# Kernel tuning notes

Hardware: AMD Instinct MI355X
Metric: run time of the kernel (lower is better)

The kernel has to match this reference:

```python
import jax, jax.numpy as jnp
import numpy as np
from jax import lax

_F1 = np.array([1., 3., 3., 1.], dtype=np.float32)
_F1 = _F1 / _F1.sum()
F2D = jnp.asarray(np.outer(_F1, _F1))  # [4,4] normalized FIR filter
LRELU_GAIN = float(np.sqrt(2.0))


def _upfirdn2d_up(x, up, pad0, pad1, gain):
    # zero-insertion upsample + pad + FIR filter (VALID depthwise conv)
    B, C, H, W = x.shape
    if up > 1:
        x = jnp.zeros((B, C, H, up, W, up), x.dtype).at[:, :, :, 0, :, 0].set(x)
        x = x.reshape(B, C, H * up, W * up)
    x = jnp.pad(x, ((0, 0), (0, 0), (pad0, pad1), (pad0, pad1)))
    k = jnp.broadcast_to((F2D * gain).astype(x.dtype), (C, 1, 4, 4))
    return lax.conv_general_dilated(x, k, (1, 1), 'VALID', feature_group_count=C)


def _affine(w, aw, ab):
    # FullyConnectedLayer: weight_gain = 1/sqrt(in_features), bias_init handled in setup
    return w @ aw.T * (1.0 / np.sqrt(aw.shape[1])) + ab


def _mod_conv(x, weight, styles, up):
    # fused modulated conv2d with demodulation, batch-as-groups trick
    B = x.shape[0]
    O, I, kh, kw = weight.shape
    w = weight[None] * styles[:, None, :, None, None]          # [B,O,I,kh,kw]
    d = lax.rsqrt(jnp.sum(jnp.square(w), axis=(2, 3, 4)) + 1e-8)  # [B,O]
    w = w * d[:, :, None, None, None]
    if up == 2:
        # conv2d_resample: FIR upsample (gain=up^2), then true conv (flipped weight)
        # padding=1, fw=4, up=2 -> px0 = 1 + (4+2-1)//2 = 3, px1 = 1 + (4-2)//2 = 2
        x = _upfirdn2d_up(x, 2, 3, 2, 4.0)
        w = w[:, :, :, ::-1, ::-1]
        pad = 'VALID'
    else:
        pad = ((kh // 2, kh // 2), (kw // 2, kw // 2))
    xr = x.reshape(1, B * I, x.shape[2], x.shape[3])
    wr = w.reshape(B * O, I, kh, kw)
    y = lax.conv_general_dilated(xr, wr, (1, 1), pad, feature_group_count=B)
    return y.reshape(B, O, y.shape[2], y.shape[3])


def _lrelu_bias(x, b, clamp=256.0):
    # bias_act: lrelu(x+b) * sqrt(2), clamp
    x = x + b[None, :, None, None]
    x = jnp.where(x >= 0, x, 0.2 * x) * LRELU_GAIN
    return jnp.clip(x, -clamp, clamp)


def setup_inputs() -> dict:
    key = jax.random.key(0)
    ks = jax.random.split(key, 12)
    B, Cin, Cout, Wd, R, IC = 8, 512, 512, 512, 64, 3
    r = R // 2
    return dict(
        x=jax.random.normal(ks[0], (B, Cin, r, r), jnp.float32),
        img=jax.random.normal(ks[1], (B, IC, r, r), jnp.float32),
        ws=jax.random.normal(ks[2], (B, 3, Wd), jnp.float32),
        a0_w=jax.random.normal(ks[3], (Cin, Wd), jnp.float32),
        a0_b=jnp.ones((Cin,), jnp.float32),
        w0=jax.random.normal(ks[4], (Cout, Cin, 3, 3), jnp.float32),
        b0=jnp.zeros((Cout,), jnp.float32),
        ns0=jnp.asarray(0.1, jnp.float32),
        nc0=jax.random.normal(ks[5], (R, R), jnp.float32),
        a1_w=jax.random.normal(ks[6], (Cout, Wd), jnp.float32),
        a1_b=jnp.ones((Cout,), jnp.float32),
        w1=jax.random.normal(ks[7], (Cout, Cout, 3, 3), jnp.float32),
        b1=jnp.zeros((Cout,), jnp.float32),
        ns1=jnp.asarray(0.1, jnp.float32),
        nc1=jax.random.normal(ks[8], (R, R), jnp.float32),
        at_w=jax.random.normal(ks[9], (Cout, Wd), jnp.float32),
        at_b=jnp.ones((Cout,), jnp.float32),
        wt=jax.random.normal(ks[10], (IC, Cout), jnp.float32),
        bt=jnp.zeros((IC,), jnp.float32),
    )


def reference(x, img, ws, a0_w, a0_b, w0, b0, ns0, nc0,
              a1_w, a1_b, w1, b1, ns1, nc1, at_w, at_b, wt, bt):
    # conv0: modulated conv, up=2, const noise, lrelu bias-act with clamp
    s0 = _affine(ws[:, 0], a0_w, a0_b)
    h = _mod_conv(x, w0, s0, up=2)
    h = h + nc0[None, None] * ns0
    h = _lrelu_bias(h, b0)
    # conv1: modulated conv, up=1
    s1 = _affine(ws[:, 1], a1_w, a1_b)
    h = _mod_conv(h, w1, s1, up=1)
    h = h + nc1[None, None] * ns1
    h = _lrelu_bias(h, b1)
    # skip architecture: upsample img (upsample2d: px0=2, px1=1, gain=4)
    img_up = _upfirdn2d_up(img, 2, 2, 1, 4.0)
    # torgb: 1x1 modulated conv, no demodulation, styles scaled by weight_gain
    st = _affine(ws[:, 2], at_w, at_b) * (1.0 / np.sqrt(wt.shape[1]))
    y = jnp.einsum('bihw,bi,oi->bohw', h, st, wt)
    y = jnp.clip(y + bt[None, :, None, None], -256.0, 256.0)
    return h, img_up + y
```

## Files before the change

### kernel.cpp

```cpp
#include <hip/hip_runtime.h>
#include <stdint.h>

typedef unsigned short u16;
typedef unsigned int   u32;

#define DEVINL __device__ __forceinline__

typedef __bf16 bf16x8 __attribute__((ext_vector_type(8)));
typedef float  f32x4  __attribute__((ext_vector_type(4)));
typedef unsigned short u16x8 __attribute__((ext_vector_type(8)));

#define RSQRT512 0.044194173824159216f
#define LRELU_G  1.4142135623730951f

DEVINL u16 f2bf(float f) {
  union { float f; u32 u; } v; v.f = f;
  u32 r = v.u + 0x7fffu + ((v.u >> 16) & 1u);
  return (u16)(r >> 16);
}
DEVINL float bf2f(u16 b) {
  union { u32 u; float f; } v; v.u = ((u32)b) << 16;
  return v.f;
}

#define AS1 __attribute__((address_space(1)))
#define AS3 __attribute__((address_space(3)))
DEVINL void gload16(const void* g, void* l) {
  __builtin_amdgcn_global_load_lds((AS1 const u32*)(uintptr_t)g,
                                   (AS3 u32*)(u32)(uintptr_t)l, 16, 0, 0);
}

__global__ __launch_bounds__(256)
void style_kernel(const float* __restrict__ wsin,
                  const float* __restrict__ a0w, const float* __restrict__ a0b,
                  const float* __restrict__ a1w, const float* __restrict__ a1b,
                  const float* __restrict__ atw, const float* __restrict__ atb,
                  float* __restrict__ s_all)
{
  int wid = threadIdx.x >> 6, lane = threadIdx.x & 63;
  int idx = blockIdx.x * 4 + wid;
  int j = idx >> 12;
  int b = (idx >> 9) & 7;
  int o = idx & 511;
  const float* A  = (j == 0) ? a0w : ((j == 1) ? a1w : atw);
  const float* Ab = (j == 0) ? a0b : ((j == 1) ? a1b : atb);
  const float* wv = wsin + (b * 3 + j) * 512;
  float p = 0.f;
  #pragma unroll
  for (int m = 0; m < 512; m += 64) p += wv[m + lane] * A[(size_t)o * 512 + m + lane];
  #pragma unroll
  for (int s = 32; s; s >>= 1) p += __shfl_xor(p, s, 64);
  if (lane == 0) {
    float v = p * RSQRT512 + Ab[o];
    if (j == 2) v *= RSQRT512;
    s_all[idx] = v;
  }
}

__global__ __launch_bounds__(256)
void demod_kernel(const float* __restrict__ w, const float* __restrict__ s_j,
                  float* __restrict__ dOut)
{
  int o = blockIdx.x;
  int t = threadIdx.x;
  __shared__ float red2[4][8];
  float part[8];
  #pragma unroll
  for (int b = 0; b < 8; ++b) part[b] = 0.f;
  #pragma unroll
  for (int hh = 0; hh < 2; ++hh) {
    int i = t + hh * 256;
    const float* wp = w + ((size_t)o * 512 + i) * 9;
    float ws = 0.f;
    #pragma unroll
    for (int k = 0; k < 9; ++k) ws += wp[k] * wp[k];
    #pragma unroll
    for (int b = 0; b < 8; ++b) {
      float sv = s_j[b * 512 + i];
      part[b] += sv * sv * ws;
    }
  }
  #pragma unroll
  for (int b = 0; b < 8; ++b)
    #pragma unroll
    for (int s = 32; s; s >>= 1) part[b] += __shfl_xor(part[b], s, 64);
  int wid = t >> 6, lane = t & 63;
  if (lane == 0) {
    #pragma unroll
    for (int b = 0; b < 8; ++b) red2[wid][b] = part[b];
  }
  __syncthreads();
  if (t < 8) {
    float d = red2[0][t] + red2[1][t] + red2[2][t] + red2[3][t];
    dOut[t * 512 + o] = 1.0f / sqrtf(d + 1e-8f);
  }
}

template <int FLIP>
__global__ __launch_bounds__(256)
void wpack_kernel(const float* __restrict__ w, const float* __restrict__ s_j,
                  const float* __restrict__ dIn, u16* __restrict__ wg)
{
  int b = blockIdx.x >> 6;
  int kq = blockIdx.x & 63;
  float sv[8];
  #pragma unroll
  for (int e = 0; e < 8; ++e) sv[e] = s_j[b * 512 + kq * 8 + e];
  int t = threadIdx.x;
  #pragma unroll 1
  for (int rep = 0; rep < 2; ++rep) {
    int o = rep * 256 + t;
    float d = dIn[b * 512 + o];
    const float* wp = w + ((size_t)o * 512 + kq * 8) * 9;
    float wv[72];
    #pragma unroll
    for (int j = 0; j < 72; ++j) wv[j] = wp[j];
    #pragma unroll
    for (int tapOut = 0; tapOut < 9; ++tapOut) {
      int ksrc = FLIP ? (8 - tapOut) : tapOut;
      u16x8 g;
      #pragma unroll
      for (int e = 0; e < 8; ++e) g[e] = f2bf(wv[e * 9 + ksrc] * sv[e] * d);
      *(u16x8*)&wg[((((size_t)(b * 9 + tapOut)) * 64 + kq) * 512 + o) * 8] = g;
    }
  }
}

__global__ __launch_bounds__(256)
void upblur_kernel(const float* __restrict__ x, u16* __restrict__ xb)
{
  int b = blockIdx.x >> 6, c8 = blockIdx.x & 63;
  __shared__ float slab[8192];
  int t = threadIdx.x;
  const float* sp = x + (((size_t)(b * 512 + c8 * 8)) << 10);
  #pragma unroll
  for (int i = 0; i < 32; ++i) slab[t + i * 256] = sp[t + i * 256];
  __syncthreads();
  u16* ob = xb + ((size_t)(b * 64 + c8)) * 34848;
  #pragma unroll 1
  for (int idx = t; idx < 4356; idx += 256) {
    int p = idx / 66;
    int q = idx - p * 66;
    int m0, m1; float wy0, wy1;
    if ((p & 1) == 0) { m0 = (p >> 1) - 1; wy0 = 0.75f; m1 = p >> 1;       wy1 = 0.25f; }
    else              { m0 = (p - 3) >> 1; wy0 = 0.25f; m1 = (p - 1) >> 1; wy1 = 0.75f; }
    int n0, n1; float wx0, wx1;
    if ((q & 1) == 0) { n0 = (q >> 1) - 1; wx0 = 0.75f; n1 = q >> 1;       wx1 = 0.25f; }
    else              { n0 = (q - 3) >> 1; wx0 = 0.25f; n1 = (q - 1) >> 1; wx1 = 0.75f; }
    bool vm0 = (unsigned)m0 < 32u, vm1 = (unsigned)m1 < 32u;
    bool vn0 = (unsigned)n0 < 32u, vn1 = (unsigned)n1 < 32u;
    float w00 = (vm0 & vn0) ? wy0 * wx0 : 0.f;
    float w01 = (vm0 & vn1) ? wy0 * wx1 : 0.f;
    float w10 = (vm1 & vn0) ? wy1 * wx0 : 0.f;
    float w11 = (vm1 & vn1) ? wy1 * wx1 : 0.f;
    int i00 = ((m0 & 31) << 5) + (n0 & 31);
    int i01 = ((m0 & 31) << 5) + (n1 & 31);
    int i10 = ((m1 & 31) << 5) + (n0 & 31);
    int i11 = ((m1 & 31) << 5) + (n1 & 31);
    u16x8 g;
    #pragma unroll
    for (int e = 0; e < 8; ++e) {
      const float* se = slab + (e << 10);
      float a = w00 * se[i00] + w01 * se[i01] + w10 * se[i10] + w11 * se[i11];
      g[e] = f2bf(a);
    }
    *(u16x8*)&ob[idx * 8] = g;
  }
}

__global__ __launch_bounds__(256)
void ringzero_kernel(u16* __restrict__ hp)
{
  u16* obase = hp + (size_t)blockIdx.x * 34848;
  int t = threadIdx.x;
  if (t < 260) {
    int y, x;
    if (t < 66)       { y = 0;       x = t; }
    else if (t < 132) { y = 65;      x = t - 66; }
    else if (t < 196) { y = t - 131; x = 0; }
    else              { y = t - 195; x = 65; }
    u16x8 z = {0, 0, 0, 0, 0, 0, 0, 0};
    *(u16x8*)&obase[(y * 66 + x) * 8] = z;
  }
}

extern __shared__ u16 dynLds[];

template <int EPI>
__global__ __launch_bounds__(1024, 4)
void conv8(const u16* __restrict__ xin,
           const u16* __restrict__ wg,
           const float* __restrict__ noise,
           const float* __restrict__ nsp,
           const float* __restrict__ bias,
           u16* __restrict__ hpOut,
           float* __restrict__ hOut)
{
  int blk = (blockIdx.x & 7) * 32 + (blockIdx.x >> 3);
  int b  = blk >> 5;
  int ot = (blk >> 4) & 1;
  int pt = blk & 15;
  int o0 = ot << 8;
  int y0 = pt << 2;

  int t = threadIdx.x;
  int w = t >> 6;
  int lane = t & 63;
  int gq = lane >> 4, r = lane & 15;
  int wm = w >> 2;
  int wn = w & 3;

  u16* Wl = dynLds;
  u16* Xl = dynLds + 32768;
  const u16* Al = (EPI == 0) ? Xl : Wl;
  const u16* Bl = (EPI == 0) ? Wl : Xl;

  f32x4 acc[4][4];
  #pragma unroll
  for (int i = 0; i < 4; ++i)
    #pragma unroll
    for (int j = 0; j < 4; ++j) acc[i][j] = (f32x4){0.f, 0.f, 0.f, 0.f};

  const u16* wbB = wg + (size_t)b * 2359296;
  const u16* xbB = xin + (size_t)b * 2230272;

  int js  = w & 7;
  int rbs = w >> 3;

  auto STAGE = [&](int tile, int pb) {
    int tap = tile >> 3;
    int ck  = tile & 7;
    int dy = (tap * 171) >> 9;
    int dx = tap - dy * 3;
    u32 base = (u32)(pb * 16384 + js * 2048 + rbs * 1024);
    const u16* wsrc = wbB + ((size_t)(tap * 64 + ck * 8 + js)) * 4096
                          + ((size_t)o0 + rbs * 128) * 8;
    const u16* xsrc = xbB + (size_t)(ck * 8 + js) * 34848;
    #pragma unroll
    for (int q = 0; q < 2; ++q) {
      gload16(wsrc + (size_t)(q * 64 + lane) * 8, Wl + base + q * 512);
      int yy = y0 + rbs * 2 + q + dy;
      gload16(xsrc + (((size_t)yy * 66) + dx + lane) * 8, Xl + base + q * 512);
    }
  };

  auto TILE = [&](int pb) {
    #pragma unroll
    for (int kk = 0; kk < 2; ++kk) {
      u32 kb = (u32)(pb * 16384) + ((u32)(kk * 4 + gq) << 11);
      bf16x8 af[4], bfr[4];
      #pragma unroll
      for (int f = 0; f < 4; ++f) {
        bfr[f] = *(const bf16x8*)&Bl[kb + ((wn * 64 + f * 16 + r) << 3)];
        af[f]  = *(const bf16x8*)&Al[kb + ((wm * 64 + f * 16 + r) << 3)];
      }
      __builtin_amdgcn_s_setprio(1);
      #pragma unroll
      for (int fa = 0; fa < 4; ++fa)
        #pragma unroll
        for (int fb = 0; fb < 4; ++fb)
          acc[fa][fb] = __builtin_amdgcn_mfma_f32_16x16x32_bf16(af[fa], bfr[fb], acc[fa][fb], 0, 0, 0);
      __builtin_amdgcn_s_setprio(0);
    }
  };

  STAGE(0, 0);
  STAGE(1, 1);
  asm volatile("s_waitcnt vmcnt(4)" ::: "memory");
  __builtin_amdgcn_sched_barrier(0);
  __builtin_amdgcn_s_barrier();
  __builtin_amdgcn_sched_barrier(0);

  int p = 0;
  #pragma unroll 1
  for (int tl = 0; tl < 72; ++tl) {
    TILE(p);
    __builtin_amdgcn_sched_barrier(0);
    __builtin_amdgcn_s_barrier();
    __builtin_amdgcn_sched_barrier(0);
    if (tl < 70) {
      STAGE(tl + 2, p);
      asm volatile("s_waitcnt vmcnt(4)" ::: "memory");
    } else if (tl == 70) {
      asm volatile("s_waitcnt vmcnt(0)" ::: "memory");
    }
    __builtin_amdgcn_sched_barrier(0);
    __builtin_amdgcn_s_barrier();
    __builtin_amdgcn_sched_barrier(0);
    p ^= 1;
  }
  __builtin_amdgcn_sched_barrier(0);

  float ns = nsp[0];
  if constexpr (EPI == 0) {
    #pragma unroll
    for (int fa = 0; fa < 4; ++fa) {
      #pragma unroll
      for (int fb = 0; fb < 4; ++fb) {
        int oo = o0 + wn * 64 + fb * 16 + r;
        float bo = bias[oo];
        #pragma unroll
        for (int v = 0; v < 4; ++v) {
          int px = wm * 64 + fa * 16 + gq * 4 + v;
          int pg = (pt << 8) + px;
          int y = pg >> 6, x2 = pg & 63;
          float val = acc[fa][fb][v] + noise[pg] * ns + bo;
          val = (val >= 0.f ? val : 0.2f * val) * LRELU_G;
          val = fminf(fmaxf(val, -256.f), 256.f);
          hpOut[((((size_t)b * 64 + (oo >> 3)) * 66 + (y + 1)) * 66 + (x2 + 1)) * 8 + (oo & 7)] = f2bf(val);
        }
      }
    }
  } else {
    #pragma unroll
    for (int fa = 0; fa < 4; ++fa) {
      #pragma unroll
      for (int fb = 0; fb < 4; ++fb) {
        int px = wn * 64 + fb * 16 + r;
        int pg = (pt << 8) + px;
        float nv = noise[pg] * ns;
        #pragma unroll
        for (int v = 0; v < 4; ++v) {
          int oo = o0 + wm * 64 + fa * 16 + gq * 4 + v;
          float val = acc[fa][fb][v] + nv + bias[oo];
          val = (val >= 0.f ? val : 0.2f * val) * LRELU_G;
          val = fminf(fmaxf(val, -256.f), 256.f);
          hOut[((size_t)(b * 512 + oo) << 12) + pg] = val;
        }
      }
    }
  }
}

__global__ __launch_bounds__(256)
void torgb_kernel(const float* __restrict__ h, const float* __restrict__ s_all,
                  const float* __restrict__ wt, const float* __restrict__ bt,
                  const float* __restrict__ img, float* __restrict__ out2)
{
  int b = blockIdx.x >> 4;
  int y = ((blockIdx.x & 15) << 2) + (threadIdx.x >> 6);
  int x = threadIdx.x & 63;
  __shared__ float stw[3][512];
  const float* st = s_all + 2 * 4096 + b * 512;
  for (int i = threadIdx.x; i < 512; i += 256) {
    float s = st[i];
    stw[0][i] = s * wt[i];
    stw[1][i] = s * wt[512 + i];
    stw[2][i] = s * wt[1024 + i];
  }
  __syncthreads();
  const float* hp = h + ((size_t)b * 512 << 12) + (y << 6) + x;
  float a0 = 0.f, a1 = 0.f, a2 = 0.f;
  #pragma unroll 8
  for (int i = 0; i < 512; ++i) {
    float v = hp[(size_t)i << 12];
    a0 += v * stw[0][i]; a1 += v * stw[1][i]; a2 += v * stw[2][i];
  }
  float accs[3] = {a0, a1, a2};
  int my0, my1; float wy0, wy1;
  if ((y & 1) == 0) { my0 = (y >> 1) - 1; wy0 = 0.25f; my1 = y >> 1;       wy1 = 0.75f; }
  else              { my0 = y >> 1;       wy0 = 0.75f; my1 = (y >> 1) + 1; wy1 = 0.25f; }
  int mx0, mx1; float wx0, wx1;
  if ((x & 1) == 0) { mx0 = (x >> 1) - 1; wx0 = 0.25f; mx1 = x >> 1;       wx1 = 0.75f; }
  else              { mx0 = x >> 1;       wx0 = 0.75f; mx1 = (x >> 1) + 1; wx1 = 0.25f; }
  bool vy0 = (unsigned)my0 < 32u, vy1 = (unsigned)my1 < 32u;
  bool vx0 = (unsigned)mx0 < 32u, vx1 = (unsigned)mx1 < 32u;
  #pragma unroll
  for (int o = 0; o < 3; ++o) {
    float yv = fminf(fmaxf(accs[o] + bt[o], -256.f), 256.f);
    const float* ib = img + ((size_t)(b * 3 + o) << 10);
    float iu = 0.f;
    if (vy0 & vx0) iu += wy0 * wx0 * ib[(my0 << 5) + mx0];
    if (vy0 & vx1) iu += wy0 * wx1 * ib[(my0 << 5) + mx1];
    if (vy1 & vx0) iu += wy1 * wx0 * ib[(my1 << 5) + mx0];
    if (vy1 & vx1) iu += wy1 * wx1 * ib[(my1 << 5) + mx1];
    out2[((size_t)(b * 3 + o) << 12) + (y << 6) + x] = iu + yv;
  }
}

extern "C" void kernel_launch(void* const* d_in, const int* in_sizes, int n_in,
                              void* d_out, int out_size, void* d_ws, size_t ws_size,
                              hipStream_t stream) {
  (void)in_sizes; (void)n_in; (void)out_size; (void)ws_size;
  const float* x   = (const float*)d_in[0];
  const float* img = (const float*)d_in[1];
  const float* ws_ = (const float*)d_in[2];
  const float* a0w = (const float*)d_in[3];
  const float* a0b = (const float*)d_in[4];
  const float* w0  = (const float*)d_in[5];
  const float* b0  = (const float*)d_in[6];
  const float* ns0 = (const float*)d_in[7];
  const float* nc0 = (const float*)d_in[8];
  const float* a1w = (const float*)d_in[9];
  const float* a1b = (const float*)d_in[10];
  const float* w1  = (const float*)d_in[11];
  const float* b1  = (const float*)d_in[12];
  const float* ns1 = (const float*)d_in[13];
  const float* nc1 = (const float*)d_in[14];
  const float* atw = (const float*)d_in[15];
  const float* atb = (const float*)d_in[16];
  const float* wt  = (const float*)d_in[17];
  const float* bt  = (const float*)d_in[18];

  char* wsp = (char*)d_ws;
  float* s_all = (float*)wsp;
  u16* wg0 = (u16*)(wsp + 49152);
  u16* wg1 = (u16*)(wsp + 49152 + 37748736ull);
  u16* xb  = (u16*)(wsp + 49152 + 2ull * 37748736);
  u16* hp  = (u16*)(wsp + 49152 + 2ull * 37748736 + 35684352);
  float* d0 = (float*)(wsp + 49152 + 2ull * 37748736 + 2ull * 35684352);
  float* d1 = (float*)(wsp + 49152 + 2ull * 37748736 + 2ull * 35684352 + 16384);

  float* h_out = (float*)d_out;
  float* out2  = (float*)d_out + 16777216;

  (void)hipFuncSetAttribute((const void*)conv8<0>,
                            hipFuncAttributeMaxDynamicSharedMemorySize, 131072);
  (void)hipFuncSetAttribute((const void*)conv8<1>,
                            hipFuncAttributeMaxDynamicSharedMemorySize, 131072);

  style_kernel<<<3072, 256, 0, stream>>>(ws_, a0w, a0b, a1w, a1b, atw, atb, s_all);
  demod_kernel<<<512, 256, 0, stream>>>(w0, s_all, d0);
  demod_kernel<<<512, 256, 0, stream>>>(w1, s_all + 4096, d1);
  wpack_kernel<1><<<512, 256, 0, stream>>>(w0, s_all, d0, wg0);
  wpack_kernel<0><<<512, 256, 0, stream>>>(w1, s_all + 4096, d1, wg1);
  upblur_kernel<<<512, 256, 0, stream>>>(x, xb);
  ringzero_kernel<<<512, 256, 0, stream>>>(hp);
  conv8<0><<<256, 1024, 131072, stream>>>(xb, wg0, nc0, ns0, b0, hp, nullptr);
  conv8<1><<<256, 1024, 131072, stream>>>(hp, wg1, nc1, ns1, b1, nullptr, h_out);
  torgb_kernel<<<128, 256, 0, stream>>>(h_out, s_all, wt, bt, img, out2);
}
```

Measured before the change: 381.5 us.

## Shrink conv block tile to 128 pixels and halve the K-step for more blocks

The implicit-GEMM conv kernel changes from 1024-thread blocks, each covering 256 pixels x 256 output channels with a K-step of 64, to 512-thread blocks covering 128 pixels x 256 channels with a K-step of 32. LDS drops from 128 KB to 48 KB, the grid doubles to 512 blocks, and the K loop doubles to 144 iterations. The intent is better occupancy and CU coverage: 512 blocks fill 256 CUs better, and several blocks can share a CU. The cost is lower weight reuse per block, meaning more global and L2 traffic for weights, and twice as many barriers per unit of work.

```diff
diff --git a/kernel.cpp b/kernel.cpp
--- a/kernel.cpp
+++ b/kernel.cpp
@@ -187,7 +187,7 @@
 extern __shared__ u16 dynLds[];
 
 template <int EPI>
-__global__ __launch_bounds__(1024, 4)
+__global__ __launch_bounds__(512, 4)
 void conv8(const u16* __restrict__ xin,
            const u16* __restrict__ wg,
            const float* __restrict__ noise,
@@ -196,24 +196,22 @@
            u16* __restrict__ hpOut,
            float* __restrict__ hOut)
 {
-  int blk = (blockIdx.x & 7) * 32 + (blockIdx.x >> 3);
-  int b  = blk >> 5;
-  int ot = (blk >> 4) & 1;
-  int pt = blk & 15;
+  int blk = (blockIdx.x & 7) * 64 + (blockIdx.x >> 3);
+  int b  = blk >> 6;
+  int ot = (blk >> 5) & 1;
+  int pt = blk & 31;
   int o0 = ot << 8;
-  int y0 = pt << 2;
+  int y0 = pt << 1;
 
   int t = threadIdx.x;
   int w = t >> 6;
   int lane = t & 63;
   int gq = lane >> 4, r = lane & 15;
-  int wm = w >> 2;
-  int wn = w & 3;
+  int w2 = w >> 2;
+  int w4 = w & 3;
 
   u16* Wl = dynLds;
-  u16* Xl = dynLds + 32768;
-  const u16* Al = (EPI == 0) ? Xl : Wl;
-  const u16* Bl = (EPI == 0) ? Wl : Xl;
+  u16* Xl = dynLds + 16384;
 
   f32x4 acc[4][4];
   #pragma unroll
@@ -224,64 +222,71 @@
   const u16* wbB = wg + (size_t)b * 2359296;
   const u16* xbB = xin + (size_t)b * 2230272;
 
-  int js  = w & 7;
-  int rbs = w >> 3;
-
   auto STAGE = [&](int tile, int pb) {
-    int tap = tile >> 3;
-    int ck  = tile & 7;
+    int tap = tile >> 4;
+    int ck  = tile & 15;
     int dy = (tap * 171) >> 9;
     int dx = tap - dy * 3;
-    u32 base = (u32)(pb * 16384 + js * 2048 + rbs * 1024);
-    const u16* wsrc = wbB + ((size_t)(tap * 64 + ck * 8 + js)) * 4096
-                          + ((size_t)o0 + rbs * 128) * 8;
-    const u16* xsrc = xbB + (size_t)(ck * 8 + js) * 34848;
-    #pragma unroll
-    for (int q = 0; q < 2; ++q) {
-      gload16(wsrc + (size_t)(q * 64 + lane) * 8, Wl + base + q * 512);
-      int yy = y0 + rbs * 2 + q + dy;
-      gload16(xsrc + (((size_t)yy * 66) + dx + lane) * 8, Xl + base + q * 512);
+    #pragma unroll
+    for (int q = 0; q < 3; ++q) {
+      int m = q * 8 + w;
+      if (m < 16) {
+        int j = m & 3, rbo = m >> 2;
+        const u16* src = wbB + ((size_t)(tap * 64 + ck * 4 + j)) * 4096
+                             + ((size_t)o0 + rbo * 64 + lane) * 8;
+        gload16(src, Wl + pb * 8192 + j * 2048 + rbo * 512);
+      } else {
+        int n = m - 16;
+        int j = n & 3, rbx = n >> 2;
+        const u16* src = xbB + (size_t)(ck * 4 + j) * 34848
+                             + (((size_t)(y0 + rbx + dy) * 66) + dx + lane) * 8;
+        gload16(src, Xl + pb * 4096 + j * 1024 + rbx * 512);
+      }
     }
   };
 
   auto TILE = [&](int pb) {
-    #pragma unroll
-    for (int kk = 0; kk < 2; ++kk) {
-      u32 kb = (u32)(pb * 16384) + ((u32)(kk * 4 + gq) << 11);
-      bf16x8 af[4], bfr[4];
+    bf16x8 af[4], bfr[4];
+    if constexpr (EPI == 0) {
       #pragma unroll
       for (int f = 0; f < 4; ++f) {
-        bfr[f] = *(const bf16x8*)&Bl[kb + ((wn * 64 + f * 16 + r) << 3)];
-        af[f]  = *(const bf16x8*)&Al[kb + ((wm * 64 + f * 16 + r) << 3)];
+        af[f]  = *(const bf16x8*)&Xl[pb * 4096 + gq * 1024 + ((w2 * 64 + f * 16 + r) << 3)];
+        bfr[f] = *(const bf16x8*)&Wl[pb * 8192 + gq * 2048 + ((w4 * 64 + f * 16 + r) << 3)];
       }
-      __builtin_amdgcn_s_setprio(1);
-      #pragma unroll
-      for (int fa = 0; fa < 4; ++fa)
-        #pragma unroll
-        for (int fb = 0; fb < 4; ++fb)
-          acc[fa][fb] = __builtin_amdgcn_mfma_f32_16x16x32_bf16(af[fa], bfr[fb], acc[fa][fb], 0, 0, 0);
-      __builtin_amdgcn_s_setprio(0);
-    }
+    } else {
+      #pragma unroll
+      for (int f = 0; f < 4; ++f) {
+        af[f]  = *(const bf16x8*)&Wl[pb * 8192 + gq * 2048 + ((w4 * 64 + f * 16 + r) << 3)];
+        bfr[f] = *(const bf16x8*)&Xl[pb * 4096 + gq * 1024 + ((w2 * 64 + f * 16 + r) << 3)];
+      }
+    }
+    __builtin_amdgcn_s_setprio(1);
+    #pragma unroll
+    for (int fa = 0; fa < 4; ++fa)
+      #pragma unroll
+      for (int fb = 0; fb < 4; ++fb)
+        acc[fa][fb] = __builtin_amdgcn_mfma_f32_16x16x32_bf16(af[fa], bfr[fb], acc[fa][fb], 0, 0, 0);
+    __builtin_amdgcn_s_setprio(0);
   };
 
   STAGE(0, 0);
   STAGE(1, 1);
-  asm volatile("s_waitcnt vmcnt(4)" ::: "memory");
+  asm volatile("s_waitcnt vmcnt(3)" ::: "memory");
   __builtin_amdgcn_sched_barrier(0);
   __builtin_amdgcn_s_barrier();
   __builtin_amdgcn_sched_barrier(0);
 
   int p = 0;
   #pragma unroll 1
-  for (int tl = 0; tl < 72; ++tl) {
+  for (int tl = 0; tl < 144; ++tl) {
     TILE(p);
     __builtin_amdgcn_sched_barrier(0);
     __builtin_amdgcn_s_barrier();
     __builtin_amdgcn_sched_barrier(0);
-    if (tl < 70) {
+    if (tl < 142) {
       STAGE(tl + 2, p);
-      asm volatile("s_waitcnt vmcnt(4)" ::: "memory");
-    } else if (tl == 70) {
+      asm volatile("s_waitcnt vmcnt(3)" ::: "memory");
+    } else if (tl == 142) {
       asm volatile("s_waitcnt vmcnt(0)" ::: "memory");
     }
     __builtin_amdgcn_sched_barrier(0);
@@ -297,12 +302,12 @@
     for (int fa = 0; fa < 4; ++fa) {
       #pragma unroll
       for (int fb = 0; fb < 4; ++fb) {
-        int oo = o0 + wn * 64 + fb * 16 + r;
+        int oo = o0 + w4 * 64 + fb * 16 + r;
         float bo = bias[oo];
         #pragma unroll
         for (int v = 0; v < 4; ++v) {
-          int px = wm * 64 + fa * 16 + gq * 4 + v;
-          int pg = (pt << 8) + px;
+          int px = w2 * 64 + fa * 16 + gq * 4 + v;
+          int pg = (pt << 7) + px;
           int y = pg >> 6, x2 = pg & 63;
           float val = acc[fa][fb][v] + noise[pg] * ns + bo;
           val = (val >= 0.f ? val : 0.2f * val) * LRELU_G;
@@ -316,12 +321,12 @@
     for (int fa = 0; fa < 4; ++fa) {
       #pragma unroll
       for (int fb = 0; fb < 4; ++fb) {
-        int px = wn * 64 + fb * 16 + r;
-        int pg = (pt << 8) + px;
+        int px = w2 * 64 + fb * 16 + r;
+        int pg = (pt << 7) + px;
         float nv = noise[pg] * ns;
         #pragma unroll
         for (int v = 0; v < 4; ++v) {
-          int oo = o0 + wm * 64 + fa * 16 + gq * 4 + v;
+          int oo = o0 + w4 * 64 + fa * 16 + gq * 4 + v;
           float val = acc[fa][fb][v] + nv + bias[oo];
           val = (val >= 0.f ? val : 0.2f * val) * LRELU_G;
           val = fminf(fmaxf(val, -256.f), 256.f);
@@ -415,9 +420,9 @@
   float* out2  = (float*)d_out + 16777216;
 
   (void)hipFuncSetAttribute((const void*)conv8<0>,
-                            hipFuncAttributeMaxDynamicSharedMemorySize, 131072);
+                            hipFuncAttributeMaxDynamicSharedMemorySize, 49152);
   (void)hipFuncSetAttribute((const void*)conv8<1>,
-                            hipFuncAttributeMaxDynamicSharedMemorySize, 131072);
+                            hipFuncAttributeMaxDynamicSharedMemorySize, 49152);
 
   style_kernel<<<3072, 256, 0, stream>>>(ws_, a0w, a0b, a1w, a1b, atw, atb, s_all);
   demod_kernel<<<512, 256, 0, stream>>>(w0, s_all, d0);
@@ -426,7 +431,7 @@
   wpack_kernel<0><<<512, 256, 0, stream>>>(w1, s_all + 4096, d1, wg1);
   upblur_kernel<<<512, 256, 0, stream>>>(x, xb);
   ringzero_kernel<<<512, 256, 0, stream>>>(hp);
-  conv8<0><<<256, 1024, 131072, stream>>>(xb, wg0, nc0, ns0, b0, hp, nullptr);
-  conv8<1><<<256, 1024, 131072, stream>>>(hp, wg1, nc1, ns1, b1, nullptr, h_out);
+  conv8<0><<<512, 512, 49152, stream>>>(xb, wg0, nc0, ns0, b0, hp, nullptr);
+  conv8<1><<<512, 512, 49152, stream>>>(hp, wg1, nc1, ns1, b1, nullptr, h_out);
   torgb_kernel<<<128, 256, 0, stream>>>(h_out, s_all, wt, bt, img, out2);
 }
```

Result: no change. 380.0 us, median of 2 (-0.4%).
